# Kernel tuning notes

Hardware: AMD Instinct MI355X
Metric: run time of the kernel (lower is better)

Reference implementation:

```python
import jax, jax.numpy as jnp
import numpy as np

B, D, T, H = 2048, 512, 16, 1024   # batch, covariate_dim, treatment_dim, mlp hidden
K, M = 50, 16                       # k_neighbors, manifold_dim


def _mlp(xt, W1, b1, W2, b2):
    # outcome model: [B, D+T] -> [B, 1]
    return jnp.tanh(xt @ W1 + b1) @ W2 + b2


def setup_inputs() -> dict:
    key = jax.random.key(0)
    k0, k1, k2, k3, k4 = jax.random.split(key, 5)
    x = jax.random.normal(k0, (B, D), dtype=jnp.float32)
    t = jax.random.normal(k1, (B, T), dtype=jnp.float32)
    perturbations = jax.random.normal(k2, (B, D), dtype=jnp.float32)
    W1 = jax.random.normal(k3, (D + T, H), dtype=jnp.float32) / np.float32(np.sqrt(D + T))
    b1 = jnp.zeros((H,), dtype=jnp.float32)
    W2 = jax.random.normal(k4, (H, 1), dtype=jnp.float32) / np.float32(np.sqrt(H))
    b2 = jnp.zeros((1,), dtype=jnp.float32)
    return {"x": x, "t": t, "perturbations": perturbations,
            "W1": W1, "b1": b1, "W2": W2, "b2": b2}


def reference(x, t, perturbations, W1, b1, W2, b2):
    # grad of sum(y) w.r.t. x (create_graph analog handled by composing jax.grad)
    def scalar_out(xx):
        return _mlp(jnp.concatenate([xx, t], axis=-1), W1, b1, W2, b2).sum()
    grad_x = jax.grad(scalar_out)(x)                      # [B, D]

    # kNN on perturbations (squared distances preserve topk-smallest ordering)
    sq = jnp.sum(perturbations * perturbations, axis=-1)  # [B]
    d2 = sq[:, None] + sq[None, :] - 2.0 * (perturbations @ perturbations.T)
    _, idx = jax.lax.top_k(-d2, K)                        # [B, K] nearest (incl. self)

    neigh = perturbations[idx]                            # [B, K, D] gather
    centered = neigh - neigh.mean(axis=1, keepdims=True)
    # batched reduced SVD: Vt has shape [B, min(K,D), D]
    _, _, Vt = jnp.linalg.svd(centered, full_matrices=False)
    basis = jnp.swapaxes(Vt[:, :M, :], 1, 2)              # [B, D, M] top-M right sing. vecs

    # projection of grad onto tangent space, summed squared norm
    coef = jnp.einsum('bdm,bd->bm', basis, grad_x)        # [B, M]
    proj = jnp.einsum('bdm,bm->bd', basis, coef)          # [B, D]
    return jnp.sum(proj * proj) / B
```

## Files before the change

### kernel.cpp

```cpp
#include <hip/hip_runtime.h>
#include <math.h>
#include <float.h>

#define B_ 2048
#define D_ 512
#define T_ 16
#define H_ 1024
#define K_ 50
#define M_ 16
#define NSWEEP 1
#define SX_STRIDE 2656
#define SLAB 128
#define SROW 136
#define FS 52

typedef __attribute__((ext_vector_type(8))) short s16x8;
typedef __attribute__((ext_vector_type(4))) float f32x4;
typedef __attribute__((ext_vector_type(2))) float f32x2;

__device__ __forceinline__ float bsum64(float v) {
  #pragma unroll
  for (int o = 1; o < 64; o <<= 1) v += __shfl_xor(v, o);
  return v;
}

__device__ __forceinline__ unsigned bf16_rne(float v) {
  union { float f; unsigned u; } a; a.f = v;
  return (a.u + 0x7FFFu + ((a.u >> 16) & 1u)) >> 16;
}
__device__ __forceinline__ float bf16_val(unsigned h) {
  union { unsigned u; float f; } a; a.u = h << 16;
  return a.f;
}
__device__ __forceinline__ void split_bf16(float v, unsigned short* h, unsigned short* l) {
  unsigned hh = bf16_rne(v);
  *h = (unsigned short)hh;
  *l = (unsigned short)bf16_rne(v - bf16_val(hh));
}

__global__ __launch_bounds__(256)
void prep_rows(const float* __restrict__ x, const float* __restrict__ t,
               const float* __restrict__ P,
               unsigned short* __restrict__ xh, unsigned short* __restrict__ xl,
               unsigned short* __restrict__ ph, unsigned short* __restrict__ pl,
               float* __restrict__ sq) {
  const int b = blockIdx.x, tid = threadIdx.x;
  for (int c = tid; c < 544; c += 256) {
    float v = 0.f;
    if (c < 512) v = x[(size_t)b * 512 + c];
    else if (c < 528) v = t[(size_t)b * 16 + (c - 512)];
    unsigned short hh, ll; split_bf16(v, &hh, &ll);
    xh[(size_t)b * 544 + c] = hh;
    xl[(size_t)b * 544 + c] = ll;
  }
  float s = 0.f;
  for (int c = tid; c < 512; c += 256) {
    float v = P[(size_t)b * 512 + c];
    s += v * v;
    unsigned short hh, ll; split_bf16(v, &hh, &ll);
    ph[(size_t)b * 512 + c] = hh;
    pl[(size_t)b * 512 + c] = ll;
  }
  __shared__ float red[4];
  s = bsum64(s);
  if ((tid & 63) == 0) red[tid >> 6] = s;
  __syncthreads();
  if (tid == 0) sq[b] = (red[0] + red[1]) + (red[2] + red[3]);
}

__global__ __launch_bounds__(256)
void conv_w1(const float* __restrict__ W1,
             unsigned short* __restrict__ th, unsigned short* __restrict__ tl,
             unsigned short* __restrict__ wh, unsigned short* __restrict__ wl) {
  __shared__ float tile[32][33];
  const int tx = threadIdx.x & 31, ty = threadIdx.x >> 5;
  const int kb = blockIdx.x * 32, hb = blockIdx.y * 32;
  #pragma unroll
  for (int j = 0; j < 4; j++) {
    int k = kb + ty + j * 8;
    float v = (k < 528) ? W1[(size_t)k * 1024 + hb + tx] : 0.f;
    tile[ty + j * 8][tx] = v;
    if (k < 528) {
      unsigned short hh, ll; split_bf16(v, &hh, &ll);
      wh[(size_t)k * 1024 + hb + tx] = hh;
      wl[(size_t)k * 1024 + hb + tx] = ll;
    }
  }
  __syncthreads();
  #pragma unroll
  for (int j = 0; j < 4; j++) {
    int hrow = hb + ty + j * 8;
    float v = tile[tx][ty + j * 8];
    unsigned short hh, ll; split_bf16(v, &hh, &ll);
    th[(size_t)hrow * 544 + kb + tx] = hh;
    tl[(size_t)hrow * 544 + kb + tx] = ll;
  }
}

template <int EPI, int PASSES>
__global__ __launch_bounds__(256)
void mfma_nt(const unsigned short* __restrict__ Ah, const unsigned short* __restrict__ Al, int lda,
             const unsigned short* __restrict__ Bh, const unsigned short* __restrict__ Bl, int ldb,
             int K, float* __restrict__ C, int ldc,
             const float* __restrict__ b1, const float* __restrict__ W2,
             unsigned short* __restrict__ acth, unsigned short* __restrict__ actl) {
  __shared__ unsigned short sAh[64 * 40], sBh[64 * 40];
  __shared__ unsigned short sAl[PASSES == 3 ? 64 * 40 : 16];
  __shared__ unsigned short sBl[PASSES == 3 ? 64 * 40 : 16];
  const int tid = threadIdx.x;
  const int lane = tid & 63, wv = tid >> 6;
  const int wm = wv >> 1, wn = wv & 1;
  const int lr = lane & 15, lq = lane >> 4;
  const int m0 = blockIdx.y * 64, n0 = blockIdx.x * 64;
  const int srow = tid >> 2, sk = (tid & 3) * 8;
  f32x4 acc[2][2];
  #pragma unroll
  for (int mt = 0; mt < 2; mt++)
    #pragma unroll
    for (int nt = 0; nt < 2; nt++)
      #pragma unroll
      for (int i = 0; i < 4; i++) acc[mt][nt][i] = 0.f;

  for (int kb = 0; kb < K; kb += 32) {
    float4 va = *(const float4*)(Ah + (size_t)(m0 + srow) * lda + kb + sk);
    float4 vc = *(const float4*)(Bh + (size_t)(n0 + srow) * ldb + kb + sk);
    float4 vb, vd;
    if (PASSES == 3) {
      vb = *(const float4*)(Al + (size_t)(m0 + srow) * lda + kb + sk);
      vd = *(const float4*)(Bl + (size_t)(n0 + srow) * ldb + kb + sk);
    }
    __syncthreads();
    *(float4*)&sAh[srow * 40 + sk] = va;
    *(float4*)&sBh[srow * 40 + sk] = vc;
    if (PASSES == 3) {
      *(float4*)&sAl[srow * 40 + sk] = vb;
      *(float4*)&sBl[srow * 40 + sk] = vd;
    }
    __syncthreads();
    s16x8 fah[2], fal[2], fbh[2], fbl[2];
    #pragma unroll
    for (int mt = 0; mt < 2; mt++) {
      const int r = wm * 32 + mt * 16 + lr;
      fah[mt] = *(const s16x8*)&sAh[r * 40 + lq * 8];
      if (PASSES == 3) fal[mt] = *(const s16x8*)&sAl[r * 40 + lq * 8];
    }
    #pragma unroll
    for (int nt = 0; nt < 2; nt++) {
      const int r = wn * 32 + nt * 16 + lr;
      fbh[nt] = *(const s16x8*)&sBh[r * 40 + lq * 8];
      if (PASSES == 3) fbl[nt] = *(const s16x8*)&sBl[r * 40 + lq * 8];
    }
    #pragma unroll
    for (int mt = 0; mt < 2; mt++)
      #pragma unroll
      for (int nt = 0; nt < 2; nt++)
        acc[mt][nt] = __builtin_amdgcn_mfma_f32_16x16x32_bf16(fah[mt], fbh[nt], acc[mt][nt], 0, 0, 0);
    if (PASSES == 3) {
      #pragma unroll
      for (int mt = 0; mt < 2; mt++)
        #pragma unroll
        for (int nt = 0; nt < 2; nt++)
          acc[mt][nt] = __builtin_amdgcn_mfma_f32_16x16x32_bf16(fah[mt], fbl[nt], acc[mt][nt], 0, 0, 0);
      #pragma unroll
      for (int mt = 0; mt < 2; mt++)
        #pragma unroll
        for (int nt = 0; nt < 2; nt++)
          acc[mt][nt] = __builtin_amdgcn_mfma_f32_16x16x32_bf16(fal[mt], fbh[nt], acc[mt][nt], 0, 0, 0);
    }
  }

  #pragma unroll
  for (int nt = 0; nt < 2; nt++) {
    const int n = n0 + wn * 32 + nt * 16 + lr;
    float bb = 0.f, ww = 0.f;
    if (EPI == 1) { bb = b1[n]; ww = W2[n]; }
    #pragma unroll
    for (int mt = 0; mt < 2; mt++) {
      #pragma unroll
      for (int r = 0; r < 4; r++) {
        const int m = m0 + wm * 32 + mt * 16 + lq * 4 + r;
        float v = acc[mt][nt][r];
        if (EPI == 0) {
          C[(size_t)m * ldc + n] = v;
        } else if (EPI == 1) {
          float z = v + bb;
          float e = __builtin_amdgcn_exp2f(fabsf(z) * -2.885390082f);
          float rc = __builtin_amdgcn_rcpf(1.f + e);
          float s = 4.f * e * rc * rc * ww;
          unsigned short hh, ll; split_bf16(s, &hh, &ll);
          acth[(size_t)m * ldc + n] = hh;
          actl[(size_t)m * ldc + n] = ll;
        } else {
          unsigned short hh, ll; split_bf16(v, &hh, &ll);
          acth[(size_t)m * ldc + n] = hh;
          actl[(size_t)m * ldc + n] = ll;
        }
      }
    }
  }
}

__global__ __launch_bounds__(256)
void sbuild_kernel(const unsigned short* __restrict__ ph, const unsigned short* __restrict__ pl,
                   const unsigned short* __restrict__ gh, const unsigned short* __restrict__ gl,
                   const int* __restrict__ idx, float* __restrict__ Sx) {
  __shared__ unsigned short sh[64 * SROW];
  __shared__ unsigned short sl[64 * SROW];
  __shared__ int ids[K_];
  const int b = blockIdx.x;
  const int tid = threadIdx.x;
  if (tid < K_) ids[tid] = idx[b * K_ + tid];
  const int lane = tid & 63, wv = tid >> 6;
  const int wm = wv >> 1, wn = wv & 1;
  const int lr = lane & 15, lq = lane >> 4;
  const int strow = tid >> 4, stk = (tid & 15) * 8;
  __syncthreads();

  f32x4 acc[2][2];
  #pragma unroll
  for (int mt = 0; mt < 2; mt++)
    #pragma unroll
    for (int nt = 0; nt < 2; nt++)
      #pragma unroll
      for (int i = 0; i < 4; i++) acc[mt][nt][i] = 0.f;

  for (int kb = 0; kb < 512; kb += SLAB) {
    __syncthreads();
    #pragma unroll
    for (int p = 0; p < 4; p++) {
      const int r = p * 16 + strow;
      if (r < 51) {
        const unsigned short* srch = (r < 50) ? ph + (size_t)ids[r] * 512 : gh + (size_t)b * 512;
        const unsigned short* srcl = (r < 50) ? pl + (size_t)ids[r] * 512 : gl + (size_t)b * 512;
        *(float4*)&sh[r * SROW + stk] = *(const float4*)(srch + kb + stk);
        *(float4*)&sl[r * SROW + stk] = *(const float4*)(srcl + kb + stk);
      }
    }
    __syncthreads();
    #pragma unroll
    for (int kk = 0; kk < SLAB; kk += 32) {
      s16x8 fah[2], fal[2], fbh[2], fbl[2];
      #pragma unroll
      for (int mt = 0; mt < 2; mt++) {
        const int r = wm * 32 + mt * 16 + lr;
        fah[mt] = *(const s16x8*)&sh[r * SROW + kk + lq * 8];
        fal[mt] = *(const s16x8*)&sl[r * SROW + kk + lq * 8];
      }
      #pragma unroll
      for (int nt = 0; nt < 2; nt++) {
        const int r = wn * 32 + nt * 16 + lr;
        fbh[nt] = *(const s16x8*)&sh[r * SROW + kk + lq * 8];
        fbl[nt] = *(const s16x8*)&sl[r * SROW + kk + lq * 8];
      }
      #pragma unroll
      for (int mt = 0; mt < 2; mt++)
        #pragma unroll
        for (int nt = 0; nt < 2; nt++)
          acc[mt][nt] = __builtin_amdgcn_mfma_f32_16x16x32_bf16(fah[mt], fbh[nt], acc[mt][nt], 0, 0, 0);
      #pragma unroll
      for (int mt = 0; mt < 2; mt++)
        #pragma unroll
        for (int nt = 0; nt < 2; nt++)
          acc[mt][nt] = __builtin_amdgcn_mfma_f32_16x16x32_bf16(fah[mt], fbl[nt], acc[mt][nt], 0, 0, 0);
      #pragma unroll
      for (int mt = 0; mt < 2; mt++)
        #pragma unroll
        for (int nt = 0; nt < 2; nt++)
          acc[mt][nt] = __builtin_amdgcn_mfma_f32_16x16x32_bf16(fal[mt], fbh[nt], acc[mt][nt], 0, 0, 0);
    }
  }

  float* Sb = Sx + (size_t)b * SX_STRIDE;
  #pragma unroll
  for (int nt = 0; nt < 2; nt++) {
    const int n = wn * 32 + nt * 16 + lr;
    #pragma unroll
    for (int mt = 0; mt < 2; mt++) {
      #pragma unroll
      for (int r = 0; r < 4; r++) {
        const int m = wm * 32 + mt * 16 + lq * 4 + r;
        if (m < 51 && n < 52) Sb[m * 52 + n] = acc[mt][nt][r];
      }
    }
  }
}

__device__ __forceinline__ unsigned fkey(float f) {
  unsigned u = __float_as_uint(f);
  return u ^ ((unsigned)((int)u >> 31) | 0x80000000u);
}

__global__ __launch_bounds__(64)
void topk_kernel(const float* __restrict__ G, const float* __restrict__ sq,
                 int* __restrict__ idx) {
  const int b = blockIdx.x, lane = threadIdx.x;
  const float* row = G + (size_t)b * 2048;
  unsigned k[32];
  #pragma unroll
  for (int i = 0; i < 32; i++) {
    const int j = i * 64 + lane;
    k[i] = fkey(sq[j] - 2.f * row[j]);
  }
  unsigned V = 0;
  bool exact = false;
  for (int bit = 31; bit >= 0; bit--) {
    const unsigned cand = V | (1u << bit);
    int cnt = 0;
    #pragma unroll
    for (int i = 0; i < 32; i++) cnt += (k[i] < cand) ? 1 : 0;
    #pragma unroll
    for (int o = 1; o < 64; o <<= 1) cnt += __shfl_xor(cnt, o);
    if (cnt == K_) { V = cand; exact = true; break; }
    if (cnt < K_ + 1) V = cand;
  }
  int base = 0;
  #pragma unroll
  for (int i = 0; i < 32; i++) {
    const bool p = (k[i] < V);
    const unsigned long long mask = __ballot(p);
    if (p) {
      const int pos = base + __popcll(mask & ((1ull << lane) - 1ull));
      idx[b * K_ + pos] = i * 64 + lane;
    }
    base += __popcll(mask);
  }
  if (!exact && base < K_) {
    #pragma unroll
    for (int i = 0; i < 32; i++) {
      if (base >= K_) break;
      const bool p = (k[i] == V);
      const unsigned long long mask = __ballot(p);
      if (p) {
        const int pos = base + __popcll(mask & ((1ull << lane) - 1ull));
        if (pos < K_) idx[b * K_ + pos] = i * 64 + lane;
      }
      base += __popcll(mask);
    }
  }
}

__global__ __launch_bounds__(64, 2)
void final_kernel(const float* __restrict__ Sx, float* __restrict__ out) {
  __shared__ float cols[64 * FS];
  const int b = blockIdx.x;
  const int lane = threadIdx.x;
  const float* Sb = Sx + (size_t)b * SX_STRIDE;
  const bool act = lane < K_;

  float q = act ? Sb[50 * 52 + lane] : 0.f;
  float qm = bsum64(q) * (1.f / K_);
  float w = act ? (q - qm) : 0.f;

  f32x2 f2[25];
  #pragma unroll
  for (int i = 0; i < 25; i++) {
    f2[i].x = act ? Sb[(2 * i) * 52 + lane] : 0.f;
    f2[i].y = act ? Sb[(2 * i + 1) * 52 + lane] : 0.f;
  }

  float cm = 0.f;
  #pragma unroll
  for (int i = 0; i < 25; i++) cm += f2[i].x + f2[i].y;
  cm *= (1.f / K_);
  float gs = bsum64(act ? cm : 0.f) * (1.f / K_);
  float cs = cm - gs;
  #pragma unroll
  for (int i = 0; i < 25; i++) {
    float r0 = __shfl(cm, 2 * i);
    float r1 = __shfl(cm, 2 * i + 1);
    if (act) { f2[i].x -= r0 + cs; f2[i].y -= r1 + cs; }
  }

  float nrm = 0.f;
  #pragma unroll
  for (int i = 0; i < 25; i++) nrm += f2[i].x * f2[i].x + f2[i].y * f2[i].y;

  f32x4 f4[13];
  #pragma unroll
  for (int k = 0; k < 12; k++) {
    f4[k].x = f2[2 * k].x;     f4[k].y = f2[2 * k].y;
    f4[k].z = f2[2 * k + 1].x; f4[k].w = f2[2 * k + 1].y;
  }
  f4[12].x = f2[24].x; f4[12].y = f2[24].y; f4[12].z = nrm; f4[12].w = w;

  float* my = &cols[lane * FS];
  if (act) {
    #pragma unroll
    for (int k = 0; k < 13; k++) *(f32x4*)&my[4 * k] = f4[k];
  }

  for (int sweep = 0; sweep < NSWEEP; sweep++) {
    int mm = (lane == 0) ? 0 : 49 - lane;
    int kkv = 0;
    for (int r = 0; r < 49; r++) {
      if (act) {
        int m = mm;
        if (lane == kkv) m = 49;
        if (lane == 49)  m = kkv;

        const float* pc = &cols[m * FS];
        f32x4 y4[13];
        #pragma unroll
        for (int k = 0; k < 13; k++) y4[k] = *(const f32x4*)&pc[4 * k];
        const float onrm = y4[12].z;
        const float yw   = y4[12].w;

        f32x4 acc4 = {0.f, 0.f, 0.f, 0.f};
        #pragma unroll
        for (int k = 0; k < 12; k++) acc4 = __builtin_elementwise_fma(f4[k], y4[k], acc4);
        acc4.x = fmaf(f4[12].x, y4[12].x, acc4.x);
        acc4.y = fmaf(f4[12].y, y4[12].y, acc4.y);
        const float dot = (acc4.x + acc4.y) + (acc4.z + acc4.w);

        const bool isp = lane < m;
        float alpha = isp ? nrm : onrm;
        float beta  = isp ? onrm : nrm;
        float tau = (beta - alpha) * 0.5f * __builtin_amdgcn_rcpf(dot);
        float sg = (tau >= 0.f) ? 1.f : -1.f;
        float s1 = __builtin_amdgcn_sqrtf(1.f + tau * tau);
        float tt = sg * __builtin_amdgcn_rcpf(fabsf(tau) + s1);
        float cc = __builtin_amdgcn_rsqf(1.f + tt * tt);
        float ssv = tt * cc;
        float sr = isp ? -ssv : ssv;
        if (fabsf(dot) < 1e-20f) { cc = 1.f; sr = 0.f; }

        f32x4 c4 = {cc, cc, cc, cc};
        f32x4 s4 = {sr, sr, sr, sr};
        #pragma unroll
        for (int k = 0; k < 13; k++)
          f4[k] = __builtin_elementwise_fma(c4, f4[k], s4 * y4[k]);
        w = cc * w + sr * yw;
        nrm = cc * cc * nrm + sr * sr * onrm + 2.f * cc * sr * dot;
        f4[12].z = nrm;
        f4[12].w = w;

        #pragma unroll
        for (int k = 0; k < 13; k++) *(f32x4*)&my[4 * k] = f4[k];
      }
      mm = (mm == 48) ? 0 : mm + 1;
      kkv += 25; if (kkv >= 49) kkv -= 49;
    }
  }

  float n2 = 0.f;
  #pragma unroll
  for (int k = 0; k < 12; k++)
    n2 += f4[k].x * f4[k].x + f4[k].y * f4[k].y + f4[k].z * f4[k].z + f4[k].w * f4[k].w;
  n2 += f4[12].x * f4[12].x + f4[12].y * f4[12].y;
  int rank = 0;
  #pragma unroll
  for (int j = 0; j < K_; j++) {
    float vj = __shfl(n2, j);
    rank += (vj > n2 || (vj == n2 && j < lane)) ? 1 : 0;
  }
  float lam = sqrtf(n2);
  float contrib = (act && rank < M_) ? (w * w / lam) : 0.f;
  contrib = bsum64(contrib);
  if (lane == 0) atomicAdd(out, contrib * (1.f / B_));
}

extern "C" void kernel_launch(void* const* d_in, const int* in_sizes, int n_in,
                              void* d_out, int out_size, void* d_ws, size_t ws_size,
                              hipStream_t stream) {
  const float* x  = (const float*)d_in[0];
  const float* t  = (const float*)d_in[1];
  const float* P  = (const float*)d_in[2];
  const float* W1 = (const float*)d_in[3];
  const float* b1 = (const float*)d_in[4];
  const float* W2 = (const float*)d_in[5];
  float* out = (float*)d_out;

  float* G    = (float*)d_ws;
  float* Sx   = (float*)d_ws;
  unsigned short* xt_h  = (unsigned short*)(G + (size_t)B_ * B_);
  unsigned short* xt_l  = xt_h  + (size_t)B_ * 544;
  unsigned short* w1t_h = xt_l  + (size_t)B_ * 544;
  unsigned short* w1t_l = w1t_h + (size_t)H_ * 544;
  unsigned short* w1_h  = w1t_l + (size_t)H_ * 544;
  unsigned short* w1_l  = w1_h  + (size_t)528 * H_;
  unsigned short* p_h   = w1_l  + (size_t)528 * H_;
  unsigned short* p_l   = p_h   + (size_t)B_ * D_;
  unsigned short* act_h = p_l   + (size_t)B_ * D_;
  unsigned short* act_l = act_h + (size_t)B_ * H_;
  unsigned short* g_h   = act_l + (size_t)B_ * H_;
  unsigned short* g_l   = g_h   + (size_t)B_ * D_;
  float* sq   = (float*)(g_l + (size_t)B_ * D_);
  int*   idx  = (int*)(sq + B_);

  hipMemsetAsync(d_out, 0, sizeof(float), stream);

  prep_rows<<<B_, 256, 0, stream>>>(x, t, P, xt_h, xt_l, p_h, p_l, sq);
  conv_w1<<<dim3(17, 32), 256, 0, stream>>>(W1, w1t_h, w1t_l, w1_h, w1_l);

  mfma_nt<1, 3><<<dim3(H_ / 64, B_ / 64), 256, 0, stream>>>(
      xt_h, xt_l, 544, w1t_h, w1t_l, 544, 544,
      nullptr, H_, b1, W2, act_h, act_l);
  mfma_nt<2, 3><<<dim3(D_ / 64, B_ / 64), 256, 0, stream>>>(
      act_h, act_l, H_, w1_h, w1_l, H_, H_,
      nullptr, D_, nullptr, nullptr, g_h, g_l);
  mfma_nt<0, 1><<<dim3(B_ / 64, B_ / 64), 256, 0, stream>>>(
      p_h, nullptr, D_, p_h, nullptr, D_, D_,
      G, B_, nullptr, nullptr, nullptr, nullptr);

  topk_kernel<<<B_, 64, 0, stream>>>(G, sq, idx);
  sbuild_kernel<<<B_, 256, 0, stream>>>(p_h, p_l, g_h, g_l, idx, Sx);
  final_kernel<<<B_, 64, 0, stream>>>(Sx, out);
}
```

Measured before the change: 254.1 us.

## Merge prep kernels, use direct global-to-LDS loads with XOR swizzle in GEMM

Fuses the row-prep and W1-conversion kernels into one launch and moves zeroing of the output into that kernel, dropping a memset and a launch. The MFMA GEMM now loads tiles straight into LDS with global_load_lds and uses an XOR-swizzled unpadded layout in place of padded rows, which cuts register staging and keeps fragment reads free of bank conflicts. The Jacobi rotation update interleaves the LDS stores with the FMAs. In exchange the GEMM loses the overlap of the next global load with the previous tile's compute, and correctness now depends on the swizzle and the lane-to-LDS address mapping of global_load_lds matching.

```diff
diff --git a/kernel.cpp b/kernel.cpp
--- a/kernel.cpp
+++ b/kernel.cpp
@@ -18,6 +18,10 @@
 typedef __attribute__((ext_vector_type(4))) float f32x4;
 typedef __attribute__((ext_vector_type(2))) float f32x2;
 
+#define GLL16(g, l) __builtin_amdgcn_global_load_lds( \
+    (const __attribute__((address_space(1))) void*)(g), \
+    (__attribute__((address_space(3))) void*)(l), 16, 0, 0)
+
 __device__ __forceinline__ float bsum64(float v) {
   #pragma unroll
   for (int o = 1; o < 64; o <<= 1) v += __shfl_xor(v, o);
@@ -39,61 +43,64 @@
 }
 
 __global__ __launch_bounds__(256)
-void prep_rows(const float* __restrict__ x, const float* __restrict__ t,
-               const float* __restrict__ P,
+void prep_conv(const float* __restrict__ x, const float* __restrict__ t,
+               const float* __restrict__ P, const float* __restrict__ W1,
                unsigned short* __restrict__ xh, unsigned short* __restrict__ xl,
                unsigned short* __restrict__ ph, unsigned short* __restrict__ pl,
-               float* __restrict__ sq) {
-  const int b = blockIdx.x, tid = threadIdx.x;
-  for (int c = tid; c < 544; c += 256) {
-    float v = 0.f;
-    if (c < 512) v = x[(size_t)b * 512 + c];
-    else if (c < 528) v = t[(size_t)b * 16 + (c - 512)];
-    unsigned short hh, ll; split_bf16(v, &hh, &ll);
-    xh[(size_t)b * 544 + c] = hh;
-    xl[(size_t)b * 544 + c] = ll;
-  }
-  float s = 0.f;
-  for (int c = tid; c < 512; c += 256) {
-    float v = P[(size_t)b * 512 + c];
-    s += v * v;
-    unsigned short hh, ll; split_bf16(v, &hh, &ll);
-    ph[(size_t)b * 512 + c] = hh;
-    pl[(size_t)b * 512 + c] = ll;
-  }
+               float* __restrict__ sq,
+               unsigned short* __restrict__ th, unsigned short* __restrict__ tl,
+               unsigned short* __restrict__ wh, unsigned short* __restrict__ wl,
+               float* __restrict__ out) {
+  __shared__ float tile[32][33];
   __shared__ float red[4];
-  s = bsum64(s);
-  if ((tid & 63) == 0) red[tid >> 6] = s;
-  __syncthreads();
-  if (tid == 0) sq[b] = (red[0] + red[1]) + (red[2] + red[3]);
-}
-
-__global__ __launch_bounds__(256)
-void conv_w1(const float* __restrict__ W1,
-             unsigned short* __restrict__ th, unsigned short* __restrict__ tl,
-             unsigned short* __restrict__ wh, unsigned short* __restrict__ wl) {
-  __shared__ float tile[32][33];
-  const int tx = threadIdx.x & 31, ty = threadIdx.x >> 5;
-  const int kb = blockIdx.x * 32, hb = blockIdx.y * 32;
-  #pragma unroll
-  for (int j = 0; j < 4; j++) {
-    int k = kb + ty + j * 8;
-    float v = (k < 528) ? W1[(size_t)k * 1024 + hb + tx] : 0.f;
-    tile[ty + j * 8][tx] = v;
-    if (k < 528) {
+  const int bid = blockIdx.x, tid = threadIdx.x;
+  if (bid < B_) {
+    const int b = bid;
+    if (b == 0 && tid == 0) out[0] = 0.f;
+    for (int c = tid; c < 544; c += 256) {
+      float v = 0.f;
+      if (c < 512) v = x[(size_t)b * 512 + c];
+      else if (c < 528) v = t[(size_t)b * 16 + (c - 512)];
       unsigned short hh, ll; split_bf16(v, &hh, &ll);
-      wh[(size_t)k * 1024 + hb + tx] = hh;
-      wl[(size_t)k * 1024 + hb + tx] = ll;
-    }
-  }
-  __syncthreads();
-  #pragma unroll
-  for (int j = 0; j < 4; j++) {
-    int hrow = hb + ty + j * 8;
-    float v = tile[tx][ty + j * 8];
-    unsigned short hh, ll; split_bf16(v, &hh, &ll);
-    th[(size_t)hrow * 544 + kb + tx] = hh;
-    tl[(size_t)hrow * 544 + kb + tx] = ll;
+      xh[(size_t)b * 544 + c] = hh;
+      xl[(size_t)b * 544 + c] = ll;
+    }
+    float s = 0.f;
+    for (int c = tid; c < 512; c += 256) {
+      float v = P[(size_t)b * 512 + c];
+      s += v * v;
+      unsigned short hh, ll; split_bf16(v, &hh, &ll);
+      ph[(size_t)b * 512 + c] = hh;
+      pl[(size_t)b * 512 + c] = ll;
+    }
+    s = bsum64(s);
+    if ((tid & 63) == 0) red[tid >> 6] = s;
+    __syncthreads();
+    if (tid == 0) sq[b] = (red[0] + red[1]) + (red[2] + red[3]);
+  } else {
+    const int cid = bid - B_;
+    const int tx = tid & 31, ty = tid >> 5;
+    const int kb = (cid % 17) * 32, hb = (cid / 17) * 32;
+    #pragma unroll
+    for (int j = 0; j < 4; j++) {
+      int k = kb + ty + j * 8;
+      float v = (k < 528) ? W1[(size_t)k * 1024 + hb + tx] : 0.f;
+      tile[ty + j * 8][tx] = v;
+      if (k < 528) {
+        unsigned short hh, ll; split_bf16(v, &hh, &ll);
+        wh[(size_t)k * 1024 + hb + tx] = hh;
+        wl[(size_t)k * 1024 + hb + tx] = ll;
+      }
+    }
+    __syncthreads();
+    #pragma unroll
+    for (int j = 0; j < 4; j++) {
+      int hrow = hb + ty + j * 8;
+      float v = tile[tx][ty + j * 8];
+      unsigned short hh, ll; split_bf16(v, &hh, &ll);
+      th[(size_t)hrow * 544 + kb + tx] = hh;
+      tl[(size_t)hrow * 544 + kb + tx] = ll;
+    }
   }
 }
 
@@ -104,15 +111,20 @@
              int K, float* __restrict__ C, int ldc,
              const float* __restrict__ b1, const float* __restrict__ W2,
              unsigned short* __restrict__ acth, unsigned short* __restrict__ actl) {
-  __shared__ unsigned short sAh[64 * 40], sBh[64 * 40];
-  __shared__ unsigned short sAl[PASSES == 3 ? 64 * 40 : 16];
-  __shared__ unsigned short sBl[PASSES == 3 ? 64 * 40 : 16];
+  __shared__ unsigned short sAh[64 * 32], sBh[64 * 32];
+  __shared__ unsigned short sAl[PASSES == 3 ? 64 * 32 : 16];
+  __shared__ unsigned short sBl[PASSES == 3 ? 64 * 32 : 16];
   const int tid = threadIdx.x;
   const int lane = tid & 63, wv = tid >> 6;
   const int wm = wv >> 1, wn = wv & 1;
   const int lr = lane & 15, lq = lane >> 4;
   const int m0 = blockIdx.y * 64, n0 = blockIdx.x * 64;
-  const int srow = tid >> 2, sk = (tid & 3) * 8;
+  const int srow = wv * 16 + (lane >> 2);
+  const int sx = (srow & 3) ^ ((srow >> 2) & 3);
+  const int gch = ((lane & 3) ^ sx) * 8;
+  unsigned short* ldsA = &sAh[wv * 512];
+  unsigned short* ldsB = &sBh[wv * 512];
+
   f32x4 acc[2][2];
   #pragma unroll
   for (int mt = 0; mt < 2; mt++)
@@ -121,34 +133,32 @@
       #pragma unroll
       for (int i = 0; i < 4; i++) acc[mt][nt][i] = 0.f;
 
+  const size_t rowA = (size_t)(m0 + srow) * lda + gch;
+  const size_t rowB = (size_t)(n0 + srow) * ldb + gch;
+
   for (int kb = 0; kb < K; kb += 32) {
-    float4 va = *(const float4*)(Ah + (size_t)(m0 + srow) * lda + kb + sk);
-    float4 vc = *(const float4*)(Bh + (size_t)(n0 + srow) * ldb + kb + sk);
-    float4 vb, vd;
+    __syncthreads();
+    GLL16(Ah + rowA + kb, ldsA);
+    GLL16(Bh + rowB + kb, ldsB);
     if (PASSES == 3) {
-      vb = *(const float4*)(Al + (size_t)(m0 + srow) * lda + kb + sk);
-      vd = *(const float4*)(Bl + (size_t)(n0 + srow) * ldb + kb + sk);
-    }
-    __syncthreads();
-    *(float4*)&sAh[srow * 40 + sk] = va;
-    *(float4*)&sBh[srow * 40 + sk] = vc;
-    if (PASSES == 3) {
-      *(float4*)&sAl[srow * 40 + sk] = vb;
-      *(float4*)&sBl[srow * 40 + sk] = vd;
+      GLL16(Al + rowA + kb, &sAl[wv * 512]);
+      GLL16(Bl + rowB + kb, &sBl[wv * 512]);
     }
     __syncthreads();
     s16x8 fah[2], fal[2], fbh[2], fbl[2];
     #pragma unroll
     for (int mt = 0; mt < 2; mt++) {
       const int r = wm * 32 + mt * 16 + lr;
-      fah[mt] = *(const s16x8*)&sAh[r * 40 + lq * 8];
-      if (PASSES == 3) fal[mt] = *(const s16x8*)&sAl[r * 40 + lq * 8];
+      const int xo = (lq ^ ((r & 3) ^ ((r >> 2) & 3))) * 8;
+      fah[mt] = *(const s16x8*)&sAh[r * 32 + xo];
+      if (PASSES == 3) fal[mt] = *(const s16x8*)&sAl[r * 32 + xo];
     }
     #pragma unroll
     for (int nt = 0; nt < 2; nt++) {
       const int r = wn * 32 + nt * 16 + lr;
-      fbh[nt] = *(const s16x8*)&sBh[r * 40 + lq * 8];
-      if (PASSES == 3) fbl[nt] = *(const s16x8*)&sBl[r * 40 + lq * 8];
+      const int xo = (lq ^ ((r & 3) ^ ((r >> 2) & 3))) * 8;
+      fbh[nt] = *(const s16x8*)&sBh[r * 32 + xo];
+      if (PASSES == 3) fbl[nt] = *(const s16x8*)&sBl[r * 32 + xo];
     }
     #pragma unroll
     for (int mt = 0; mt < 2; mt++)
@@ -426,16 +436,18 @@
 
         f32x4 c4 = {cc, cc, cc, cc};
         f32x4 s4 = {sr, sr, sr, sr};
-        #pragma unroll
-        for (int k = 0; k < 13; k++)
+        const float w_new   = cc * w + sr * yw;
+        const float nrm_new = cc * cc * nrm + sr * sr * onrm + 2.f * cc * sr * dot;
+        #pragma unroll
+        for (int k = 0; k < 12; k++) {
           f4[k] = __builtin_elementwise_fma(c4, f4[k], s4 * y4[k]);
-        w = cc * w + sr * yw;
-        nrm = cc * cc * nrm + sr * sr * onrm + 2.f * cc * sr * dot;
+          *(f32x4*)&my[4 * k] = f4[k];
+        }
+        f4[12] = __builtin_elementwise_fma(c4, f4[12], s4 * y4[12]);
+        w = w_new; nrm = nrm_new;
         f4[12].z = nrm;
         f4[12].w = w;
-
-        #pragma unroll
-        for (int k = 0; k < 13; k++) *(f32x4*)&my[4 * k] = f4[k];
+        *(f32x4*)&my[48] = f4[12];
       }
       mm = (mm == 48) ? 0 : mm + 1;
       kkv += 25; if (kkv >= 49) kkv -= 49;
@@ -487,10 +499,8 @@
   float* sq   = (float*)(g_l + (size_t)B_ * D_);
   int*   idx  = (int*)(sq + B_);
 
-  hipMemsetAsync(d_out, 0, sizeof(float), stream);
-
-  prep_rows<<<B_, 256, 0, stream>>>(x, t, P, xt_h, xt_l, p_h, p_l, sq);
-  conv_w1<<<dim3(17, 32), 256, 0, stream>>>(W1, w1t_h, w1t_l, w1_h, w1_l);
+  prep_conv<<<B_ + 544, 256, 0, stream>>>(x, t, P, W1, xt_h, xt_l, p_h, p_l, sq,
+                                          w1t_h, w1t_l, w1_h, w1_l, out);
 
   mfma_nt<1, 3><<<dim3(H_ / 64, B_ / 64), 256, 0, stream>>>(
       xt_h, xt_l, 544, w1t_h, w1t_l, 544, 544,
```

Result: faster. 248.4 us (-2.2%).
